# Kernel tuning notes

Measured on AMD Instinct MI355X. Metric: run time of the kernel, lower is better.

Reference implementation:

```python
import jax, jax.numpy as jnp
import numpy as np

B, S, D, H = 2, 2048, 1024, 16
DK = D // H

def setup_inputs() -> dict:
    key = jax.random.key(0)
    ks = jax.random.split(key, 11)
    scale = 1.0 / np.sqrt(D)
    inp = {
        'Q': jax.random.normal(ks[0], (B, S, D), jnp.float32),
        'K': jax.random.normal(ks[1], (B, S, D), jnp.float32),
        'V': jax.random.normal(ks[2], (B, S, D), jnp.float32),
        'Wq': jax.random.normal(ks[3], (D, D), jnp.float32) * scale,
        'bq': jax.random.normal(ks[4], (D,), jnp.float32) * 0.01,
        'Wk': jax.random.normal(ks[5], (D, D), jnp.float32) * scale,
        'bk': jax.random.normal(ks[6], (D,), jnp.float32) * 0.01,
        'Wv': jax.random.normal(ks[7], (D, D), jnp.float32) * scale,
        'bv': jax.random.normal(ks[8], (D,), jnp.float32) * 0.01,
        'Wo': jax.random.normal(ks[9], (D, D), jnp.float32) * scale,
        'bo': jax.random.normal(ks[10], (D,), jnp.float32) * 0.01,
    }
    return inp

def reference(Q, K, V, Wq, bq, Wk, bk, Wv, bv, Wo, bo):
    bs = Q.shape[0]
    # projections (torch Linear: x @ W.T + b), reshape to [b, h, s, d_k]
    q = (Q @ Wq.T + bq).reshape(bs, -1, H, DK).transpose(0, 2, 1, 3)
    k = (K @ Wk.T + bk).reshape(bs, -1, H, DK).transpose(0, 2, 1, 3)
    v = (V @ Wv.T + bv).reshape(bs, -1, H, DK).transpose(0, 2, 1, 3)
    # scaled dot-product attention (no mask, dropout p=0)
    scores = jnp.einsum('bhqd,bhkd->bhqk', q, k) / np.sqrt(DK).astype(np.float32)
    attn = jax.nn.softmax(scores, axis=-1)
    ctx = jnp.einsum('bhqk,bhkd->bhqd', attn, v)
    concat = ctx.transpose(0, 2, 1, 3).reshape(bs, -1, D)
    return concat @ Wo.T + bo
```

## Files before the change

kernel.cpp:

```cpp
#include <hip/hip_runtime.h>
#include <hip/hip_bf16.h>
#include <stdint.h>

#define B_  2
#define S_  2048
#define D_  1024
#define H_  16
#define DK_ 64
#define M_  (B_ * S_)

#define QSCALE 0.18033688011112042f

typedef __attribute__((ext_vector_type(4)))  float f32x4;
typedef __attribute__((ext_vector_type(16))) float f32x16;
typedef __attribute__((ext_vector_type(8)))  short bf16x8;

__device__ __forceinline__ unsigned short f2bf(float f) {
    union { float f; unsigned u; } a; a.f = f;
    unsigned u = a.u;
    unsigned r = (u + 0x7fffu + ((u >> 16) & 1u)) >> 16;
    return (unsigned short)r;
}
__device__ __forceinline__ unsigned pk2(float lo, float hi) {
    union { float f; unsigned u; } a, b; a.f = lo; b.f = hi;
    unsigned ra = a.u + 0x7fffu + ((a.u >> 16) & 1u);
    unsigned rb = b.u + 0x7fffu + ((b.u >> 16) & 1u);
    return __builtin_amdgcn_perm(rb, ra, 0x07060302u);
}
__device__ __forceinline__ unsigned pk2f(float lo, float hi) {
    union { float f; unsigned u; } a, b; a.f = lo; b.f = hi;
    return __builtin_amdgcn_perm(b.u + 0x8000u, a.u + 0x8000u, 0x07060302u);
}

__device__ __forceinline__ void gload16(const void* g, void* l) {
    __builtin_amdgcn_global_load_lds(
        (const __attribute__((address_space(1))) void*)g,
        (__attribute__((address_space(3))) void*)l, 16, 0, 0);
}

__global__ __launch_bounds__(256) void cvt_all(
    const float* __restrict__ p0, const float* __restrict__ p1,
    const float* __restrict__ p2, const float* __restrict__ p3,
    const float* __restrict__ p4, const float* __restrict__ p5,
    const float* __restrict__ p6,
    unsigned short* __restrict__ o0, unsigned short* __restrict__ o1,
    unsigned short* __restrict__ o2, unsigned short* __restrict__ o3,
    unsigned short* __restrict__ o4, unsigned short* __restrict__ o5,
    unsigned short* __restrict__ o6) {
    const int y = blockIdx.y;
    if (y >= 3 && blockIdx.x >= 512) return;
    const float* in = (y == 0) ? p0 : (y == 1) ? p1 : (y == 2) ? p2 :
                      (y == 3) ? p3 : (y == 4) ? p4 : (y == 5) ? p5 : p6;
    unsigned short* out = (y == 0) ? o0 : (y == 1) ? o1 : (y == 2) ? o2 :
                          (y == 3) ? o3 : (y == 4) ? o4 : (y == 5) ? o5 : o6;
    const int i = blockIdx.x * 256 + threadIdx.x;
    const float4* p = (const float4*)in + (size_t)i * 2;
    float4 u = p[0], v = p[1];
    union { unsigned us[4]; bf16x8 v; } o;
    o.us[0] = pk2(u.x, u.y); o.us[1] = pk2(u.z, u.w);
    o.us[2] = pk2(v.x, v.y); o.us[3] = pk2(v.z, v.w);
    *((bf16x8*)out + i) = o.v;
}

__device__ __forceinline__ void gemm128_core(const unsigned short* __restrict__ A,
                                             const unsigned short* __restrict__ Bw,
                                             unsigned short* As, unsigned short* Bs,
                                             int brow, int bcol, f32x4 (&acc)[4][4]) {
    constexpr int K = D_;
    const int t = threadIdx.x;
    const int l = t & 63;
    const int l15 = l & 15, l4 = l >> 4;
    const int wr = (t >> 6) >> 1, wc = (t >> 6) & 1;

    const unsigned short* Ap = A + (size_t)(brow + (t >> 2)) * K + (t & 3) * 8;
    const unsigned short* Bp = Bw + (size_t)(bcol + (t >> 2)) * K + (t & 3) * 8;
    unsigned short* AsT = As + t * 8;
    unsigned short* BsT = Bs + t * 8;

    for (int k0 = 0; k0 < K; k0 += 32) {
        __syncthreads();
        gload16(Ap + k0, AsT);
        gload16(Ap + 64 * K + k0, AsT + 2048);
        gload16(Bp + k0, BsT);
        gload16(Bp + 64 * K + k0, BsT + 2048);
        __syncthreads();

        bf16x8 af[4], bfv[4];
#pragma unroll
        for (int m = 0; m < 4; m++)
            af[m] = *(const bf16x8*)(As + (wr * 64 + m * 16 + l15) * 32 + l4 * 8);
#pragma unroll
        for (int n = 0; n < 4; n++)
            bfv[n] = *(const bf16x8*)(Bs + (wc * 64 + n * 16 + l15) * 32 + l4 * 8);
#pragma unroll
        for (int m = 0; m < 4; m++)
#pragma unroll
            for (int n = 0; n < 4; n++)
                acc[m][n] = __builtin_amdgcn_mfma_f32_16x16x32_bf16(af[m], bfv[n],
                                                                    acc[m][n], 0, 0, 0);
    }
}

__global__ __launch_bounds__(256) void gemm_qkv(
    const unsigned short* __restrict__ xq, const unsigned short* __restrict__ xk,
    const unsigned short* __restrict__ xv,
    const unsigned short* __restrict__ wq, const unsigned short* __restrict__ wk,
    const unsigned short* __restrict__ wv,
    const float* __restrict__ bq, const float* __restrict__ bk,
    const float* __restrict__ bv,
    unsigned short* __restrict__ oq, unsigned short* __restrict__ ok,
    unsigned short* __restrict__ ov) {
    __shared__ unsigned short As[128 * 32];
    __shared__ unsigned short Bs[128 * 32];

    const int bid = blockIdx.x;
    const int wg = (bid & 7) * 96 + (bid >> 3);
    const int bx = wg & 7, by = (wg >> 3) & 31, z = wg >> 8;

    const unsigned short* A  = (z == 0) ? xq : (z == 1) ? xk : xv;
    const unsigned short* Bw = (z == 0) ? wq : (z == 1) ? wk : wv;
    const float* bias        = (z == 0) ? bq : (z == 1) ? bk : bv;
    unsigned short* out      = (z == 0) ? oq : (z == 1) ? ok : ov;

    const int brow = by * 128;
    const int bcol = bx * 128;
    const f32x4 zf = {0.0f, 0.0f, 0.0f, 0.0f};
    f32x4 acc[4][4];
#pragma unroll
    for (int i = 0; i < 4; i++)
#pragma unroll
        for (int j = 0; j < 4; j++) acc[i][j] = zf;

    gemm128_core(A, Bw, As, Bs, brow, bcol, acc);

    const int t = threadIdx.x;
    const int l = t & 63;
    const int l15 = l & 15, l4 = l >> 4;
    const int wr = (t >> 6) >> 1, wc = (t >> 6) & 1;
    const float scale = (z == 0) ? QSCALE : 1.0f;

#pragma unroll
    for (int n = 0; n < 4; n++) {
        const int col = bcol + wc * 64 + n * 16 + l15;
        const float bia = bias[col];
        const int h = col >> 6, dk = col & 63;
#pragma unroll
        for (int m = 0; m < 4; m++) {
            const int row0 = brow + wr * 64 + m * 16 + l4 * 4;
            const int b = row0 >> 11, s0 = row0 & (S_ - 1);
            if (z != 2) {
#pragma unroll
                for (int r = 0; r < 4; r++) {
                    float v = (acc[m][n][r] + bia) * scale;
                    out[((size_t)((b * H_ + h) * S_ + (s0 + r))) * DK_ + dk] = f2bf(v);
                }
            } else {
                const int st_ = s0 >> 7, sl = s0 & 127;
                const int g = (sl >> 6) & 1, c = (sl >> 4) & 3;
                const int j2 = (sl >> 2) & 3;
                const int sig = ((j2 & 1) << 1) | (j2 >> 1);
                uint2 o;
                o.x = pk2(acc[m][n][0] + bia, acc[m][n][1] + bia);
                o.y = pk2(acc[m][n][2] + bia, acc[m][n][3] + bia);
                *(uint2*)((char*)out +
                          (((((size_t)(b * H_ + h) * 16 + st_) * 2 + g) * 4 + c) * 64 + dk) * 32 +
                          sig * 8) = o;
            }
        }
    }
}

__global__ __launch_bounds__(256) void gemm_out(const unsigned short* __restrict__ A,
                                                const unsigned short* __restrict__ Bw,
                                                const float* __restrict__ bias,
                                                float* __restrict__ out) {
    __shared__ unsigned short As[128 * 32];
    __shared__ unsigned short Bs[128 * 32];

    const int bid = blockIdx.x;
    const int wg = (bid & 7) * 32 + (bid >> 3);
    const int bx = wg & 7, by = wg >> 3;

    const int brow = by * 128;
    const int bcol = bx * 128;
    const f32x4 zf = {0.0f, 0.0f, 0.0f, 0.0f};
    f32x4 acc[4][4];
#pragma unroll
    for (int i = 0; i < 4; i++)
#pragma unroll
        for (int j = 0; j < 4; j++) acc[i][j] = zf;

    gemm128_core(A, Bw, As, Bs, brow, bcol, acc);

    const int t = threadIdx.x;
    const int l = t & 63;
    const int l15 = l & 15, l4 = l >> 4;
    const int wr = (t >> 6) >> 1, wc = (t >> 6) & 1;
#pragma unroll
    for (int n = 0; n < 4; n++) {
        const int col = bcol + wc * 64 + n * 16 + l15;
        const float bia = bias[col];
#pragma unroll
        for (int m = 0; m < 4; m++) {
            const int row0 = brow + wr * 64 + m * 16 + l4 * 4;
#pragma unroll
            for (int r = 0; r < 4; r++)
                out[(size_t)(row0 + r) * D_ + col] = acc[m][n][r] + bia;
        }
    }
}

__global__ __launch_bounds__(512, 4) void attn_kernel(const unsigned short* __restrict__ qh,
                                                      const unsigned short* __restrict__ kh,
                                                      const unsigned short* __restrict__ vimg,
                                                      unsigned short* __restrict__ ctx) {
    __shared__ unsigned short smem[2][16384];
    char* smb = (char*)smem;

    const int t = threadIdx.x;
    const int w = t >> 6, l = t & 63;
    const int l31 = l & 31, hi = l >> 5;
    const int hi16 = hi * 16;
    const int grp = w >> 2;
    const int qs  = w & 3;

    const int bid = blockIdx.x;
    const int bh = (bid & 7) * 4 + ((bid >> 3) & 3);
    const int qt = bid >> 5;
    const int b = bh >> 4, h = bh & 15;

    const unsigned short* qg = qh + (size_t)bh * S_ * DK_;
    const unsigned short* kg = kh + (size_t)bh * S_ * DK_;

    const int q0 = qt * 128 + qs * 32;

    bf16x8 qf[4];
#pragma unroll
    for (int kc = 0; kc < 4; kc++)
        qf[kc] = *(const bf16x8*)(qg + (size_t)(q0 + l31) * DK_ + kc * 16 + hi * 8);

    const f32x16 zf16 = {0.0f};
    f32x16 acc0 = zf16, acc1 = zf16;
    float lpart = 0.0f;

    const int kc_ = t >> 7, key_ = (t >> 1) & 63, hi_ = t & 1;
    const unsigned short* ksrc = kg + key_ * DK_ + kc_ * 16 + hi_ * 8;
    const unsigned short* vsrc = vimg + (size_t)bh * (16 * 8192) + t * 8;

    {
        char* kd = smb + t * 16;
        gload16(ksrc, kd);
        gload16(ksrc + 4096, kd + 8192);
        gload16(vsrc, kd + 16384);
        gload16(vsrc + 4096, kd + 16384 + 8192);
        ksrc += 8192; vsrc += 8192;
    }
    __syncthreads();

    unsigned roff = grp * 8192 + l31 * 32 + hi16;
    unsigned pd = 32768 + (unsigned)t * 16;

    for (int j = 0; j < 16; ++j) {
        if (j < 15) {
            gload16(ksrc, smb + pd);
            gload16(ksrc + 4096, smb + pd + 8192);
            gload16(vsrc, smb + pd + 16384);
            gload16(vsrc + 4096, smb + pd + 16384 + 8192);
            ksrc += 8192; vsrc += 8192;
        }

        const char* Kb = smb + roff;

        f32x16 st0, st1;
        __builtin_amdgcn_s_setprio(1);
        {
            bf16x8 k0 = *(const bf16x8*)(Kb);
            bf16x8 k1 = *(const bf16x8*)(Kb + 1024);
            st0 = __builtin_amdgcn_mfma_f32_32x32x16_bf16(k0, qf[0], zf16, 0, 0, 0);
            st1 = __builtin_amdgcn_mfma_f32_32x32x16_bf16(k1, qf[0], zf16, 0, 0, 0);
        }
#pragma unroll
        for (int kc = 1; kc < 4; kc++) {
            bf16x8 k0 = *(const bf16x8*)(Kb + kc * 2048);
            bf16x8 k1 = *(const bf16x8*)(Kb + kc * 2048 + 1024);
            st0 = __builtin_amdgcn_mfma_f32_32x32x16_bf16(k0, qf[kc], st0, 0, 0, 0);
            st1 = __builtin_amdgcn_mfma_f32_32x32x16_bf16(k1, qf[kc], st1, 0, 0, 0);
        }
        __builtin_amdgcn_s_setprio(0);

#pragma unroll
        for (int i = 0; i < 16; i++) st0[i] = __builtin_amdgcn_exp2f(st0[i]);
#pragma unroll
        for (int i = 0; i < 16; i++) st1[i] = __builtin_amdgcn_exp2f(st1[i]);

        float sv[8];
#pragma unroll
        for (int i = 0; i < 8; i++) sv[i] = (st0[i] + st0[i + 8]) + (st1[i] + st1[i + 8]);
#pragma unroll
        for (int s = 4; s >= 1; s >>= 1)
#pragma unroll
            for (int i = 0; i < s; i++) sv[i] += sv[i + s];
        lpart += sv[0];

        bf16x8 pf[4];
        {
            union { unsigned u[4]; bf16x8 v; } pu;
            pu.u[0] = pk2f(st0[0], st0[1]);   pu.u[1] = pk2f(st0[2], st0[3]);
            pu.u[2] = pk2f(st0[4], st0[5]);   pu.u[3] = pk2f(st0[6], st0[7]);
            pf[0] = pu.v;
            pu.u[0] = pk2f(st0[8], st0[9]);   pu.u[1] = pk2f(st0[10], st0[11]);
            pu.u[2] = pk2f(st0[12], st0[13]); pu.u[3] = pk2f(st0[14], st0[15]);
            pf[1] = pu.v;
            pu.u[0] = pk2f(st1[0], st1[1]);   pu.u[1] = pk2f(st1[2], st1[3]);
            pu.u[2] = pk2f(st1[4], st1[5]);   pu.u[3] = pk2f(st1[6], st1[7]);
            pf[2] = pu.v;
            pu.u[0] = pk2f(st1[8], st1[9]);   pu.u[1] = pk2f(st1[10], st1[11]);
            pu.u[2] = pk2f(st1[12], st1[13]); pu.u[3] = pk2f(st1[14], st1[15]);
            pf[3] = pu.v;
        }

        const char* Vb = smb + roff;
        __builtin_amdgcn_s_setprio(1);
#pragma unroll
        for (int c = 0; c < 4; c++) {
            bf16x8 v0 = *(const bf16x8*)(Vb + 16384 + c * 2048);
            bf16x8 v1 = *(const bf16x8*)(Vb + 16384 + c * 2048 + 1024);
            acc0 = __builtin_amdgcn_mfma_f32_32x32x16_bf16(v0, pf[c], acc0, 0, 0, 0);
            acc1 = __builtin_amdgcn_mfma_f32_32x32x16_bf16(v1, pf[c], acc1, 0, 0, 0);
        }
        __builtin_amdgcn_s_setprio(0);

        if (j < 15) __syncthreads();
        roff ^= 32768;
        pd ^= 32768;
    }

    lpart += __shfl_xor(lpart, 32);
    __syncthreads();
    char* ab = smb + qs * 8192 + l31 * 256;
    const int msw = (l31 & 7) << 4;
    if (grp == 1) {
#pragma unroll
        for (int jj = 0; jj < 4; jj++) {
            f32x4 x0 = {acc0[4 * jj], acc0[4 * jj + 1], acc0[4 * jj + 2], acc0[4 * jj + 3]};
            f32x4 x1 = {acc1[4 * jj], acc1[4 * jj + 1], acc1[4 * jj + 2], acc1[4 * jj + 3]};
            *(f32x4*)(ab + ((jj * 32 + hi16) ^ msw)) = x0;
            *(f32x4*)(ab + (128 + ((jj * 32 + hi16) ^ msw))) = x1;
        }
        if (hi == 0)
            *(float*)(smb + 32768 + qs * 128 + l31 * 4) = lpart;
    }
    __syncthreads();
    if (grp == 0) {
        const float lB = *(const float*)(smb + 32768 + qs * 128 + l31 * 4);
        const float inv = 1.0f / (lpart + lB);
        unsigned short* op = ctx + ((size_t)b * S_ + (q0 + l31)) * D_ + h * 64;
#pragma unroll
        for (int jj = 0; jj < 4; jj++) {
            f32x4 b0 = *(const f32x4*)(ab + ((jj * 32 + hi16) ^ msw));
            f32x4 b1 = *(const f32x4*)(ab + (128 + ((jj * 32 + hi16) ^ msw)));
            uint2 o;
            o.x = pk2f((acc0[4 * jj + 0] + b0[0]) * inv, (acc0[4 * jj + 1] + b0[1]) * inv);
            o.y = pk2f((acc0[4 * jj + 2] + b0[2]) * inv, (acc0[4 * jj + 3] + b0[3]) * inv);
            *(uint2*)(op + jj * 8 + hi * 4) = o;
            o.x = pk2f((acc1[4 * jj + 0] + b1[0]) * inv, (acc1[4 * jj + 1] + b1[1]) * inv);
            o.y = pk2f((acc1[4 * jj + 2] + b1[2]) * inv, (acc1[4 * jj + 3] + b1[3]) * inv);
            *(uint2*)(op + 32 + jj * 8 + hi * 4) = o;
        }
    }
}

extern "C" void kernel_launch(void* const* d_in, const int* in_sizes, int n_in,
                              void* d_out, int out_size, void* d_ws, size_t ws_size,
                              hipStream_t stream) {
    const float* Q  = (const float*)d_in[0];
    const float* K  = (const float*)d_in[1];
    const float* V  = (const float*)d_in[2];
    const float* Wq = (const float*)d_in[3];
    const float* bq = (const float*)d_in[4];
    const float* Wk = (const float*)d_in[5];
    const float* bk = (const float*)d_in[6];
    const float* Wv = (const float*)d_in[7];
    const float* bv = (const float*)d_in[8];
    const float* Wo = (const float*)d_in[9];
    const float* bo = (const float*)d_in[10];

    const size_t NX = (size_t)M_ * D_;
    const size_t NW = (size_t)D_ * D_;

    unsigned short* ws = (unsigned short*)d_ws;
    unsigned short* xq  = ws; ws += NX;
    unsigned short* xk  = ws; ws += NX;
    unsigned short* xv  = ws; ws += NX;
    unsigned short* wqb = ws; ws += NW;
    unsigned short* wkb = ws; ws += NW;
    unsigned short* wvb = ws; ws += NW;
    unsigned short* wob = ws; ws += NW;
    unsigned short* qhb = ws; ws += NX;
    unsigned short* khb = ws; ws += NX;
    unsigned short* vip = ws; ws += NX;
    unsigned short* ctx = ws; ws += NX;

    cvt_all<<<dim3(2048, 7), 256, 0, stream>>>(Q, K, V, Wq, Wk, Wv, Wo,
                                               xq, xk, xv, wqb, wkb, wvb, wob);

    gemm_qkv<<<dim3(768), 256, 0, stream>>>(
        xq, xk, xv, wqb, wkb, wvb, bq, bk, bv, qhb, khb, vip);

    attn_kernel<<<dim3(512), 512, 0, stream>>>(qhb, khb, vip, ctx);

    gemm_out<<<dim3(256), 256, 0, stream>>>(ctx, wob, bo, (float*)d_out);
}
```

Baseline: 117.3 us.

## Double-buffer LDS tiles in the shared GEMM core to overlap loads with MFMA

Replaces the single A/B shared-memory tile pair with two 16 KB buffers in one 32 KB region. The next K-slice is prefetched into the alternate buffer while MFMAs run on the current one, and the loop drops from two barriers per iteration to one. This is meant to hide global-to-LDS latency in both the QKV and output projection GEMMs. In exchange it doubles LDS use per block, which could lower occupancy.

```diff
diff --git a/kernel.cpp b/kernel.cpp
--- a/kernel.cpp
+++ b/kernel.cpp
@@ -64,7 +64,7 @@
 
 __device__ __forceinline__ void gemm128_core(const unsigned short* __restrict__ A,
                                              const unsigned short* __restrict__ Bw,
-                                             unsigned short* As, unsigned short* Bs,
+                                             char* sm,
                                              int brow, int bcol, f32x4 (&acc)[4][4]) {
     constexpr int K = D_;
     const int t = threadIdx.x;
@@ -74,30 +74,43 @@
 
     const unsigned short* Ap = A + (size_t)(brow + (t >> 2)) * K + (t & 3) * 8;
     const unsigned short* Bp = Bw + (size_t)(bcol + (t >> 2)) * K + (t & 3) * 8;
-    unsigned short* AsT = As + t * 8;
-    unsigned short* BsT = Bs + t * 8;
-
+
+    {
+        char* d = sm + t * 16;
+        gload16(Ap, d);
+        gload16(Ap + 64 * K, d + 4096);
+        gload16(Bp, d + 8192);
+        gload16(Bp + 64 * K, d + 12288);
+    }
+    __syncthreads();
+
+    unsigned sbuf = 0;
     for (int k0 = 0; k0 < K; k0 += 32) {
-        __syncthreads();
-        gload16(Ap + k0, AsT);
-        gload16(Ap + 64 * K + k0, AsT + 2048);
-        gload16(Bp + k0, BsT);
-        gload16(Bp + 64 * K + k0, BsT + 2048);
-        __syncthreads();
-
+        if (k0 + 32 < K) {
+            char* d = sm + (sbuf ^ 16384u) + t * 16;
+            gload16(Ap + k0 + 32, d);
+            gload16(Ap + 64 * K + k0 + 32, d + 4096);
+            gload16(Bp + k0 + 32, d + 8192);
+            gload16(Bp + 64 * K + k0 + 32, d + 12288);
+        }
+
+        const char* Ab = sm + sbuf;
         bf16x8 af[4], bfv[4];
 #pragma unroll
         for (int m = 0; m < 4; m++)
-            af[m] = *(const bf16x8*)(As + (wr * 64 + m * 16 + l15) * 32 + l4 * 8);
+            af[m] = *(const bf16x8*)(Ab + (wr * 64 + m * 16 + l15) * 64 + l4 * 16);
 #pragma unroll
         for (int n = 0; n < 4; n++)
-            bfv[n] = *(const bf16x8*)(Bs + (wc * 64 + n * 16 + l15) * 32 + l4 * 8);
+            bfv[n] = *(const bf16x8*)(Ab + 8192 + (wc * 64 + n * 16 + l15) * 64 + l4 * 16);
 #pragma unroll
         for (int m = 0; m < 4; m++)
 #pragma unroll
             for (int n = 0; n < 4; n++)
                 acc[m][n] = __builtin_amdgcn_mfma_f32_16x16x32_bf16(af[m], bfv[n],
                                                                     acc[m][n], 0, 0, 0);
+
+        if (k0 + 32 < K) __syncthreads();
+        sbuf ^= 16384u;
     }
 }
 
@@ -110,8 +123,7 @@
     const float* __restrict__ bv,
     unsigned short* __restrict__ oq, unsigned short* __restrict__ ok,
     unsigned short* __restrict__ ov) {
-    __shared__ unsigned short As[128 * 32];
-    __shared__ unsigned short Bs[128 * 32];
+    __shared__ char sm[32768];
 
     const int bid = blockIdx.x;
     const int wg = (bid & 7) * 96 + (bid >> 3);
@@ -131,7 +143,7 @@
 #pragma unroll
         for (int j = 0; j < 4; j++) acc[i][j] = zf;
 
-    gemm128_core(A, Bw, As, Bs, brow, bcol, acc);
+    gemm128_core(A, Bw, sm, brow, bcol, acc);
 
     const int t = threadIdx.x;
     const int l = t & 63;
@@ -174,8 +186,7 @@
                                                 const unsigned short* __restrict__ Bw,
                                                 const float* __restrict__ bias,
                                                 float* __restrict__ out) {
-    __shared__ unsigned short As[128 * 32];
-    __shared__ unsigned short Bs[128 * 32];
+    __shared__ char sm[32768];
 
     const int bid = blockIdx.x;
     const int wg = (bid & 7) * 32 + (bid >> 3);
@@ -190,7 +201,7 @@
 #pragma unroll
         for (int j = 0; j < 4; j++) acc[i][j] = zf;
 
-    gemm128_core(A, Bw, As, Bs, brow, bcol, acc);
+    gemm128_core(A, Bw, sm, brow, bcol, acc);
 
     const int t = threadIdx.x;
     const int l = t & 63;
```

Measured after the change: 111.4 us. 5.0% less time.

## Double-buffer GEMM LDS tiles and shrink tiles for more blocks

Applied to the files above, without the earlier changes.

Replaces the single-buffered 128x128 GEMM core with a double-buffered loop that prefetches the next K-slice into a second LDS buffer while computing the current one, using one barrier per iteration. The QKV projection tile shrinks to 128x64 (1536 blocks) and the output projection to 64x64 (1024 blocks) to fill more CUs, with launch bounds raised for occupancy. The LDS layout is changed to a k-chunk-major arrangement. Smaller tiles lower arithmetic intensity and raise global/L2 traffic in exchange for better parallelism and latency hiding.

```diff
diff --git a/kernel.cpp b/kernel.cpp
--- a/kernel.cpp
+++ b/kernel.cpp
@@ -62,46 +62,60 @@
     *((bf16x8*)out + i) = o.v;
 }
 
-__device__ __forceinline__ void gemm128_core(const unsigned short* __restrict__ A,
-                                             const unsigned short* __restrict__ Bw,
-                                             unsigned short* As, unsigned short* Bs,
-                                             int brow, int bcol, f32x4 (&acc)[4][4]) {
+__device__ __forceinline__ void gemm_core_128x64(const unsigned short* __restrict__ A,
+                                                 const unsigned short* __restrict__ Bw,
+                                                 char* sm, int brow, int bcol,
+                                                 f32x4 (&acc)[4][2]) {
     constexpr int K = D_;
     const int t = threadIdx.x;
     const int l = t & 63;
     const int l15 = l & 15, l4 = l >> 4;
     const int wr = (t >> 6) >> 1, wc = (t >> 6) & 1;
 
-    const unsigned short* Ap = A + (size_t)(brow + (t >> 2)) * K + (t & 3) * 8;
-    const unsigned short* Bp = Bw + (size_t)(bcol + (t >> 2)) * K + (t & 3) * 8;
-    unsigned short* AsT = As + t * 8;
-    unsigned short* BsT = Bs + t * 8;
-
+    const unsigned short* As1 = A + (size_t)(brow + (t & 127)) * K + (t >> 7) * 8;
+    const unsigned short* As2 = As1 + 16;
+    const unsigned short* Bs1 = Bw + (size_t)(bcol + (t & 63)) * K + (t >> 6) * 8;
+    const unsigned dln = (unsigned)t * 16;
+
+    {
+        char* d = sm + dln;
+        gload16(As1, d);
+        gload16(As2, d + 4096);
+        gload16(Bs1, d + 8192);
+    }
+    __syncthreads();
+
+    const unsigned abase = (unsigned)(l4 * 128 + wr * 64 + l15) * 16;
+    const unsigned bbase = 8192u + (unsigned)(l4 * 64 + wc * 32 + l15) * 16;
+
+    char* cur = sm;
+    char* nxt = sm + 12288;
     for (int k0 = 0; k0 < K; k0 += 32) {
-        __syncthreads();
-        gload16(Ap + k0, AsT);
-        gload16(Ap + 64 * K + k0, AsT + 2048);
-        gload16(Bp + k0, BsT);
-        gload16(Bp + 64 * K + k0, BsT + 2048);
-        __syncthreads();
-
-        bf16x8 af[4], bfv[4];
+        if (k0 + 32 < K) {
+            char* d = nxt + dln;
+            gload16(As1 + k0 + 32, d);
+            gload16(As2 + k0 + 32, d + 4096);
+            gload16(Bs1 + k0 + 32, d + 8192);
+        }
+
+        bf16x8 af[4], bfv[2];
+#pragma unroll
+        for (int m = 0; m < 4; m++) af[m] = *(const bf16x8*)(cur + abase + m * 256);
+#pragma unroll
+        for (int n = 0; n < 2; n++) bfv[n] = *(const bf16x8*)(cur + bbase + n * 256);
 #pragma unroll
         for (int m = 0; m < 4; m++)
-            af[m] = *(const bf16x8*)(As + (wr * 64 + m * 16 + l15) * 32 + l4 * 8);
-#pragma unroll
-        for (int n = 0; n < 4; n++)
-            bfv[n] = *(const bf16x8*)(Bs + (wc * 64 + n * 16 + l15) * 32 + l4 * 8);
-#pragma unroll
-        for (int m = 0; m < 4; m++)
-#pragma unroll
-            for (int n = 0; n < 4; n++)
+#pragma unroll
+            for (int n = 0; n < 2; n++)
                 acc[m][n] = __builtin_amdgcn_mfma_f32_16x16x32_bf16(af[m], bfv[n],
                                                                     acc[m][n], 0, 0, 0);
-    }
-}
-
-__global__ __launch_bounds__(256) void gemm_qkv(
+
+        if (k0 + 32 < K) __syncthreads();
+        char* tmp = cur; cur = nxt; nxt = tmp;
+    }
+}
+
+__global__ __launch_bounds__(256, 6) void gemm_qkv(
     const unsigned short* __restrict__ xq, const unsigned short* __restrict__ xk,
     const unsigned short* __restrict__ xv,
     const unsigned short* __restrict__ wq, const unsigned short* __restrict__ wk,
@@ -110,12 +124,12 @@
     const float* __restrict__ bv,
     unsigned short* __restrict__ oq, unsigned short* __restrict__ ok,
     unsigned short* __restrict__ ov) {
-    __shared__ unsigned short As[128 * 32];
-    __shared__ unsigned short Bs[128 * 32];
+    __shared__ char sm[24576];
 
     const int bid = blockIdx.x;
-    const int wg = (bid & 7) * 96 + (bid >> 3);
-    const int bx = wg & 7, by = (wg >> 3) & 31, z = wg >> 8;
+    const int wg = (bid & 7) * 192 + (bid >> 3);
+    const int z = wg >> 9;
+    const int bx = wg & 15, by = (wg >> 4) & 31;
 
     const unsigned short* A  = (z == 0) ? xq : (z == 1) ? xk : xv;
     const unsigned short* Bw = (z == 0) ? wq : (z == 1) ? wk : wv;
@@ -123,15 +137,13 @@
     unsigned short* out      = (z == 0) ? oq : (z == 1) ? ok : ov;
 
     const int brow = by * 128;
-    const int bcol = bx * 128;
+    const int bcol = bx * 64;
     const f32x4 zf = {0.0f, 0.0f, 0.0f, 0.0f};
-    f32x4 acc[4][4];
-#pragma unroll
-    for (int i = 0; i < 4; i++)
-#pragma unroll
-        for (int j = 0; j < 4; j++) acc[i][j] = zf;
-
-    gemm128_core(A, Bw, As, Bs, brow, bcol, acc);
+    f32x4 acc[4][2];
+#pragma unroll
+    for (int i = 0; i < 4; i++) { acc[i][0] = zf; acc[i][1] = zf; }
+
+    gemm_core_128x64(A, Bw, sm, brow, bcol, acc);
 
     const int t = threadIdx.x;
     const int l = t & 63;
@@ -140,8 +152,8 @@
     const float scale = (z == 0) ? QSCALE : 1.0f;
 
 #pragma unroll
-    for (int n = 0; n < 4; n++) {
-        const int col = bcol + wc * 64 + n * 16 + l15;
+    for (int n = 0; n < 2; n++) {
+        const int col = bcol + wc * 32 + n * 16 + l15;
         const float bia = bias[col];
         const int h = col >> 6, dk = col & 63;
 #pragma unroll
@@ -170,39 +182,75 @@
     }
 }
 
-__global__ __launch_bounds__(256) void gemm_out(const unsigned short* __restrict__ A,
-                                                const unsigned short* __restrict__ Bw,
-                                                const float* __restrict__ bias,
-                                                float* __restrict__ out) {
-    __shared__ unsigned short As[128 * 32];
-    __shared__ unsigned short Bs[128 * 32];
+__global__ __launch_bounds__(256, 6) void gemm_out(const unsigned short* __restrict__ A,
+                                                   const unsigned short* __restrict__ Bw,
+                                                   const float* __restrict__ bias,
+                                                   float* __restrict__ out) {
+    constexpr int K = D_;
+    __shared__ char sm[16384];
 
     const int bid = blockIdx.x;
-    const int wg = (bid & 7) * 32 + (bid >> 3);
-    const int bx = wg & 7, by = wg >> 3;
-
-    const int brow = by * 128;
-    const int bcol = bx * 128;
-    const f32x4 zf = {0.0f, 0.0f, 0.0f, 0.0f};
-    f32x4 acc[4][4];
-#pragma unroll
-    for (int i = 0; i < 4; i++)
-#pragma unroll
-        for (int j = 0; j < 4; j++) acc[i][j] = zf;
-
-    gemm128_core(A, Bw, As, Bs, brow, bcol, acc);
+    const int wg = (bid & 7) * 128 + (bid >> 3);
+    const int bx = wg & 15, by = wg >> 4;
+
+    const int brow = by * 64;
+    const int bcol = bx * 64;
 
     const int t = threadIdx.x;
     const int l = t & 63;
     const int l15 = l & 15, l4 = l >> 4;
     const int wr = (t >> 6) >> 1, wc = (t >> 6) & 1;
-#pragma unroll
-    for (int n = 0; n < 4; n++) {
-        const int col = bcol + wc * 64 + n * 16 + l15;
+
+    const f32x4 zf = {0.0f, 0.0f, 0.0f, 0.0f};
+    f32x4 acc[2][2];
+    acc[0][0] = zf; acc[0][1] = zf; acc[1][0] = zf; acc[1][1] = zf;
+
+    const unsigned short* As1 = A + (size_t)(brow + (t & 63)) * K + (t >> 6) * 8;
+    const unsigned short* Bs1 = Bw + (size_t)(bcol + (t & 63)) * K + (t >> 6) * 8;
+    const unsigned dln = (unsigned)t * 16;
+
+    {
+        char* d = sm + dln;
+        gload16(As1, d);
+        gload16(Bs1, d + 4096);
+    }
+    __syncthreads();
+
+    const unsigned abase = (unsigned)(l4 * 64 + wr * 32 + l15) * 16;
+    const unsigned bbase = 4096u + (unsigned)(l4 * 64 + wc * 32 + l15) * 16;
+
+    char* cur = sm;
+    char* nxt = sm + 8192;
+    for (int k0 = 0; k0 < K; k0 += 32) {
+        if (k0 + 32 < K) {
+            char* d = nxt + dln;
+            gload16(As1 + k0 + 32, d);
+            gload16(Bs1 + k0 + 32, d + 4096);
+        }
+
+        bf16x8 af[2], bfv[2];
+#pragma unroll
+        for (int m = 0; m < 2; m++) af[m] = *(const bf16x8*)(cur + abase + m * 256);
+#pragma unroll
+        for (int n = 0; n < 2; n++) bfv[n] = *(const bf16x8*)(cur + bbase + n * 256);
+#pragma unroll
+        for (int m = 0; m < 2; m++)
+#pragma unroll
+            for (int n = 0; n < 2; n++)
+                acc[m][n] = __builtin_amdgcn_mfma_f32_16x16x32_bf16(af[m], bfv[n],
+                                                                    acc[m][n], 0, 0, 0);
+
+        if (k0 + 32 < K) __syncthreads();
+        char* tmp = cur; cur = nxt; nxt = tmp;
+    }
+
+#pragma unroll
+    for (int n = 0; n < 2; n++) {
+        const int col = bcol + wc * 32 + n * 16 + l15;
         const float bia = bias[col];
 #pragma unroll
-        for (int m = 0; m < 4; m++) {
-            const int row0 = brow + wr * 64 + m * 16 + l4 * 4;
+        for (int m = 0; m < 2; m++) {
+            const int row0 = brow + wr * 32 + m * 16 + l4 * 4;
 #pragma unroll
             for (int r = 0; r < 4; r++)
                 out[(size_t)(row0 + r) * D_ + col] = acc[m][n][r] + bia;
@@ -404,10 +452,10 @@
     cvt_all<<<dim3(2048, 7), 256, 0, stream>>>(Q, K, V, Wq, Wk, Wv, Wo,
                                                xq, xk, xv, wqb, wkb, wvb, wob);
 
-    gemm_qkv<<<dim3(768), 256, 0, stream>>>(
+    gemm_qkv<<<dim3(1536), 256, 0, stream>>>(
         xq, xk, xv, wqb, wkb, wvb, bq, bk, bv, qhb, khb, vip);
 
     attn_kernel<<<dim3(512), 512, 0, stream>>>(qhb, khb, vip, ctx);
 
-    gemm_out<<<dim3(256), 256, 0, stream>>>(ctx, wob, bo, (float*)d_out);
-}
+    gemm_out<<<dim3(1024), 256, 0, stream>>>(ctx, wob, bo, (float*)d_out);
+}
```

Result: slower. 166.3 us (+41.7%).

## Triple-buffer LDS in shared GEMM core with async prefetch two stages ahead

Applied to the files above, without the earlier changes.

Replaces the single-buffered, two-barrier K loop in the shared 128x128 GEMM core with a three-stage LDS ring buffer. Global-to-LDS loads for step k+2 are issued while step k computes, using explicit vmcnt waits and a single barrier per iteration. The LDS layout is also changed to a k-chunk-major arrangement, which gives different bank access patterns for the fragment reads. LDS use per block rises from 16KB to 48KB, which may reduce occupancy.

```diff
diff --git a/kernel.cpp b/kernel.cpp
--- a/kernel.cpp
+++ b/kernel.cpp
@@ -64,40 +64,59 @@
 
 __device__ __forceinline__ void gemm128_core(const unsigned short* __restrict__ A,
                                              const unsigned short* __restrict__ Bw,
-                                             unsigned short* As, unsigned short* Bs,
-                                             int brow, int bcol, f32x4 (&acc)[4][4]) {
+                                             char* sm, int brow, int bcol,
+                                             f32x4 (&acc)[4][4]) {
     constexpr int K = D_;
     const int t = threadIdx.x;
     const int l = t & 63;
     const int l15 = l & 15, l4 = l >> 4;
     const int wr = (t >> 6) >> 1, wc = (t >> 6) & 1;
 
-    const unsigned short* Ap = A + (size_t)(brow + (t >> 2)) * K + (t & 3) * 8;
-    const unsigned short* Bp = Bw + (size_t)(bcol + (t >> 2)) * K + (t & 3) * 8;
-    unsigned short* AsT = As + t * 8;
-    unsigned short* BsT = Bs + t * 8;
-
-    for (int k0 = 0; k0 < K; k0 += 32) {
-        __syncthreads();
-        gload16(Ap + k0, AsT);
-        gload16(Ap + 64 * K + k0, AsT + 2048);
-        gload16(Bp + k0, BsT);
-        gload16(Bp + 64 * K + k0, BsT + 2048);
-        __syncthreads();
-
+    const unsigned short* Ap = A + (size_t)(brow + (t & 127)) * K + (t >> 7) * 8;
+    const unsigned short* Bp = Bw + (size_t)(bcol + (t & 127)) * K + (t >> 7) * 8;
+    const unsigned dln = (unsigned)t * 16;
+
+    auto STAGE = [&](int k0, int buf) {
+        char* d = sm + buf * 16384 + dln;
+        gload16(Ap + k0, d);
+        gload16(Ap + k0 + 16, d + 4096);
+        gload16(Bp + k0, d + 8192);
+        gload16(Bp + k0 + 16, d + 12288);
+    };
+
+    STAGE(0, 0);
+    STAGE(32, 1);
+
+    const unsigned abase = (unsigned)((l4 * 128 + wr * 64 + l15) * 16);
+    const unsigned bbase = 8192u + (unsigned)((l4 * 128 + wc * 64 + l15) * 16);
+
+    int cur = 0;
+    for (int ki = 0; ki < K / 32; ++ki) {
+        if (ki + 1 < K / 32)
+            asm volatile("s_waitcnt vmcnt(4) lgkmcnt(0)\n\ts_barrier" ::: "memory");
+        else
+            asm volatile("s_waitcnt vmcnt(0) lgkmcnt(0)\n\ts_barrier" ::: "memory");
+        __builtin_amdgcn_sched_barrier(0);
+
+        if (ki + 2 < K / 32) {
+            int tgt = cur + 2; if (tgt >= 3) tgt -= 3;
+            STAGE((ki + 2) * 32, tgt);
+        }
+
+        const char* Ab = sm + cur * 16384;
         bf16x8 af[4], bfv[4];
 #pragma unroll
-        for (int m = 0; m < 4; m++)
-            af[m] = *(const bf16x8*)(As + (wr * 64 + m * 16 + l15) * 32 + l4 * 8);
-#pragma unroll
-        for (int n = 0; n < 4; n++)
-            bfv[n] = *(const bf16x8*)(Bs + (wc * 64 + n * 16 + l15) * 32 + l4 * 8);
+        for (int m = 0; m < 4; m++) af[m] = *(const bf16x8*)(Ab + abase + m * 256);
+#pragma unroll
+        for (int n = 0; n < 4; n++) bfv[n] = *(const bf16x8*)(Ab + bbase + n * 256);
 #pragma unroll
         for (int m = 0; m < 4; m++)
 #pragma unroll
             for (int n = 0; n < 4; n++)
                 acc[m][n] = __builtin_amdgcn_mfma_f32_16x16x32_bf16(af[m], bfv[n],
                                                                     acc[m][n], 0, 0, 0);
+
+        cur = (cur + 1 == 3) ? 0 : cur + 1;
     }
 }
 
@@ -110,8 +129,7 @@
     const float* __restrict__ bv,
     unsigned short* __restrict__ oq, unsigned short* __restrict__ ok,
     unsigned short* __restrict__ ov) {
-    __shared__ unsigned short As[128 * 32];
-    __shared__ unsigned short Bs[128 * 32];
+    __shared__ char sm[49152];
 
     const int bid = blockIdx.x;
     const int wg = (bid & 7) * 96 + (bid >> 3);
@@ -131,7 +149,7 @@
 #pragma unroll
         for (int j = 0; j < 4; j++) acc[i][j] = zf;
 
-    gemm128_core(A, Bw, As, Bs, brow, bcol, acc);
+    gemm128_core(A, Bw, sm, brow, bcol, acc);
 
     const int t = threadIdx.x;
     const int l = t & 63;
@@ -174,8 +192,7 @@
                                                 const unsigned short* __restrict__ Bw,
                                                 const float* __restrict__ bias,
                                                 float* __restrict__ out) {
-    __shared__ unsigned short As[128 * 32];
-    __shared__ unsigned short Bs[128 * 32];
+    __shared__ char sm[49152];
 
     const int bid = blockIdx.x;
     const int wg = (bid & 7) * 32 + (bid >> 3);
@@ -190,7 +207,7 @@
 #pragma unroll
         for (int j = 0; j < 4; j++) acc[i][j] = zf;
 
-    gemm128_core(A, Bw, As, Bs, brow, bcol, acc);
+    gemm128_core(A, Bw, sm, brow, bcol, acc);
 
     const int t = threadIdx.x;
     const int l = t & 63;
```

Measured after the change: 133.2 us. 1.14x slower.
